# Kernel tuning notes

Hardware: AMD Instinct MI355X
Metric: run time of the kernel (lower is better)

The kernel has to match this reference:

```python
import jax, jax.numpy as jnp
import numpy as np

N_NODES = 50000
N_EDGES = 800000
VOCAB = 500
IN_DIM = 128
HID = 128
OUT_DIM = 64
N_GRAPHS = 512


def setup_inputs() -> dict:
    key = jax.random.key(0)
    ks = jax.random.split(key, 12)
    s = 0.05
    return {
        "emb": jax.random.normal(ks[0], (VOCAB, IN_DIM), jnp.float32) * s,
        "w1a": jax.random.normal(ks[1], (HID, IN_DIM), jnp.float32) * s,
        "b1a": jnp.zeros((HID,), jnp.float32),
        "w1b": jax.random.normal(ks[2], (HID, HID), jnp.float32) * s,
        "b1b": jnp.zeros((HID,), jnp.float32),
        "w2a": jax.random.normal(ks[3], (HID, HID), jnp.float32) * s,
        "b2a": jnp.zeros((HID,), jnp.float32),
        "w2b": jax.random.normal(ks[4], (HID, HID), jnp.float32) * s,
        "b2b": jnp.zeros((HID,), jnp.float32),
        "fc_w": jax.random.normal(ks[5], (OUT_DIM, HID), jnp.float32) * s,
        "fc_b": jnp.zeros((OUT_DIM,), jnp.float32),
        "x_idx": jax.random.randint(ks[6], (N_NODES,), 0, VOCAB, jnp.int32),
        "edge_index": jax.random.randint(ks[7], (2, N_EDGES), 0, N_NODES, jnp.int32),
        "batch": jnp.sort(jax.random.randint(ks[8], (N_NODES,), 0, N_GRAPHS, jnp.int32)),
    }


def gin_conv(x, wa, ba, wb, bb, src, dst):
    # GINConv with eps=0: MLP(x + sum_{j->i} x_j)
    agg = jax.ops.segment_sum(x[src], dst, num_segments=N_NODES)  # [N, d]
    h = x + agg
    h = jax.nn.relu(h @ wa.T + ba)
    return h @ wb.T + bb


def reference(emb, w1a, b1a, w1b, b1b, w2a, b2a, w2b, b2b, fc_w, fc_b,
              x_idx, edge_index, batch):
    src, dst = edge_index[0], edge_index[1]
    x = emb[x_idx]  # [N, IN_DIM] embedding lookup
    x = jax.nn.relu(gin_conv(x, w1a, b1a, w1b, b1b, src, dst))
    x = jax.nn.relu(gin_conv(x, w2a, b2a, w2b, b2b, src, dst))
    # global mean pool over graphs
    sums = jax.ops.segment_sum(x, batch, num_segments=N_GRAPHS)  # [G, HID]
    cnt = jax.ops.segment_sum(jnp.ones((N_NODES,), x.dtype), batch, num_segments=N_GRAPHS)
    pooled = sums / jnp.maximum(cnt, 1.0)[:, None]
    return pooled @ fc_w.T + fc_b  # [G, OUT_DIM]
```

## Files before the change

### kernel.cpp

```cpp
#include <hip/hip_runtime.h>

#define N_NODES 50000
#define N_EDGES 800000
#define DIM 128
#define NGRAPH 512
#define ODIM 64
#define VOCAB 500
#define NBKT 391
#define NB2 128
#define EPB2 (N_EDGES / NB2)
#define CAP 4096

typedef __attribute__((ext_vector_type(8))) short bf16x8;
typedef __attribute__((ext_vector_type(4))) short bf16x4;
typedef __attribute__((ext_vector_type(4))) float f32x4;

__device__ inline unsigned short f2bf(float f) {
  unsigned u = __builtin_bit_cast(unsigned, f);
  return (unsigned short)((u + 0x7fffu + ((u >> 16) & 1u)) >> 16);
}
__device__ inline float bf2f(unsigned short h) {
  unsigned u = ((unsigned)h) << 16;
  return __builtin_bit_cast(float, u);
}

__global__ __launch_bounds__(256) void prep_kernel(
    const float* __restrict__ emb,
    const float* __restrict__ w1a, const float* __restrict__ w1b,
    const float* __restrict__ w2a, const float* __restrict__ w2b,
    unsigned short* __restrict__ embb, unsigned short* __restrict__ wbf) {
  int u = blockIdx.x * 256 + threadIdx.x;
  const float* src;
  unsigned short* dst;
  if (u < VOCAB * 16) {
    src = emb + (size_t)u * 8;
    dst = embb + (size_t)u * 8;
  } else {
    int v = u - VOCAB * 16;
    if (v >= 4 * 2048) return;
    int m = v >> 11, loc = v & 2047;
    const float* w = (m == 0) ? w1a : (m == 1) ? w1b : (m == 2) ? w2a : w2b;
    src = w + (size_t)loc * 8;
    dst = wbf + (size_t)v * 8;
  }
  f32x4 a = ((const f32x4*)src)[0], b = ((const f32x4*)src)[1];
  bf16x8 o;
  #pragma unroll
  for (int e = 0; e < 4; ++e) {
    o[e] = (short)f2bf(a[e]);
    o[4 + e] = (short)f2bf(b[e]);
  }
  *(bf16x8*)dst = o;
}

__global__ __launch_bounds__(512) void bkt_hist_kernel(
    const int* __restrict__ ei, unsigned* __restrict__ HB) {
  __shared__ unsigned cnt[NBKT];
  int t = threadIdx.x, b = blockIdx.x;
  for (int i = t; i < NBKT; i += 512) cnt[i] = 0;
  __syncthreads();
  int base = b * EPB2;
  for (int i = t; i < EPB2; i += 512)
    atomicAdd(&cnt[(unsigned)ei[N_EDGES + base + i] >> 7], 1u);
  __syncthreads();
  for (int i = t; i < NBKT; i += 512) HB[(size_t)b * NBKT + i] = cnt[i];
}

__global__ __launch_bounds__(512) void bkt_scatter_kernel(
    const int* __restrict__ ei, const unsigned* __restrict__ HB,
    unsigned* __restrict__ eb) {
  __shared__ unsigned cur[NBKT];
  __shared__ unsigned wsum[8];
  int t = threadIdx.x, b = blockIdx.x;
  int lane = t & 63, wid = t >> 6;
  unsigned pre = 0, tot = 0;
  if (t < NBKT) {
    for (int bb = 0; bb < NB2; ++bb) {
      unsigned h = HB[(size_t)bb * NBKT + t];
      pre += (bb < b) ? h : 0u;
      tot += h;
    }
  }
  unsigned s = tot;
  #pragma unroll
  for (int d = 1; d < 64; d <<= 1) {
    unsigned u = __shfl_up(s, d, 64);
    if (lane >= d) s += u;
  }
  if (lane == 63) wsum[wid] = s;
  __syncthreads();
  if (wid == 0) {
    unsigned ws = (lane < 8) ? wsum[lane] : 0u;
    #pragma unroll
    for (int d = 1; d < 8; d <<= 1) {
      unsigned u = __shfl_up(ws, d, 64);
      if (lane >= d) ws += u;
    }
    if (lane < 8) wsum[lane] = ws;
  }
  __syncthreads();
  unsigned base = s - tot + (wid ? wsum[wid - 1] : 0u);
  if (t < NBKT) cur[t] = base + pre;
  __syncthreads();
  int ebase = b * EPB2;
  for (int i = t; i < EPB2; i += 512) {
    int sn = ei[ebase + i];
    unsigned d = (unsigned)ei[N_EDGES + ebase + i];
    unsigned pos = atomicAdd(&cur[d >> 7], 1u);
    eb[pos] = ((d & 127u) << 16) | (unsigned)sn;
  }
}

__global__ __launch_bounds__(512) void sort_bucket_kernel(
    const unsigned* __restrict__ HB, const unsigned* __restrict__ eb,
    int* __restrict__ srt, int* __restrict__ row) {
  __shared__ unsigned stage[CAP];
  __shared__ unsigned short sorted[CAP];
  __shared__ unsigned hist[128], cur[128];
  __shared__ unsigned wtot, wsum[8];
  __shared__ int sbound[2];
  int t = threadIdx.x, bkt = blockIdx.x;
  int lane = t & 63, wid = t >> 6;
  unsigned tot = 0;
  if (t < NBKT)
    for (int bb = 0; bb < NB2; ++bb) tot += HB[(size_t)bb * NBKT + t];
  unsigned s = tot;
  #pragma unroll
  for (int d = 1; d < 64; d <<= 1) {
    unsigned u = __shfl_up(s, d, 64);
    if (lane >= d) s += u;
  }
  if (lane == 63) wsum[wid] = s;
  __syncthreads();
  if (wid == 0) {
    unsigned ws = (lane < 8) ? wsum[lane] : 0u;
    #pragma unroll
    for (int d = 1; d < 8; d <<= 1) {
      unsigned u = __shfl_up(ws, d, 64);
      if (lane >= d) ws += u;
    }
    if (lane < 8) wsum[lane] = ws;
  }
  __syncthreads();
  unsigned base = s - tot + (wid ? wsum[wid - 1] : 0u);
  if (t == bkt) { sbound[0] = (int)base; sbound[1] = (int)(base + tot); }
  if (t < 128) hist[t] = 0;
  if (bkt == 0 && t == 0) row[N_NODES] = N_EDGES;
  __syncthreads();
  int bs = sbound[0];
  int cnt = sbound[1] - bs;
  if (cnt > CAP) cnt = CAP;
  for (int i = t; i < cnt; i += 512) {
    unsigned e = eb[bs + i];
    stage[i] = e;
    atomicAdd(&hist[e >> 16], 1u);
  }
  __syncthreads();
  if (t < 128) {
    unsigned v = hist[t], ss = v;
    #pragma unroll
    for (int d = 1; d < 64; d <<= 1) {
      unsigned u = __shfl_up(ss, d, 64);
      if (lane >= d) ss += u;
    }
    if (t == 63) wtot = ss;
    cur[t] = ss - v;
  }
  __syncthreads();
  if (t < 128) {
    unsigned e0 = cur[t] + (t >= 64 ? wtot : 0u);
    cur[t] = e0;
    int n = bkt * 128 + t;
    if (n < N_NODES) row[n] = bs + (int)e0;
  }
  __syncthreads();
  for (int i = t; i < cnt; i += 512) {
    unsigned e = stage[i];
    unsigned r = atomicAdd(&cur[e >> 16], 1u);
    sorted[r] = (unsigned short)(e & 0xFFFFu);
  }
  __syncthreads();
  for (int i = t; i < cnt; i += 512) srt[bs + i] = (int)sorted[i];
}

__global__ __launch_bounds__(256) void agg_emb_kernel(
    const unsigned short* __restrict__ embb, const int* __restrict__ xidx,
    const int* __restrict__ row, const int* __restrict__ srt,
    unsigned short* __restrict__ xa) {
  int n = blockIdx.x * 16 + (threadIdx.x >> 4);
  int c = threadIdx.x & 15;
  int lo = row[n], hi = row[n + 1];
  bf16x8 sv = *(const bf16x8*)(embb + (size_t)xidx[n] * DIM + c * 8);
  float a[8];
  #pragma unroll
  for (int e = 0; e < 8; ++e) a[e] = bf2f((unsigned short)sv[e]);
  int k = lo;
  for (; k + 8 <= hi; k += 8) {
    bf16x8 w[8];
    #pragma unroll
    for (int q = 0; q < 8; ++q)
      w[q] = *(const bf16x8*)(embb + (size_t)xidx[srt[k + q]] * DIM + c * 8);
    #pragma unroll
    for (int q = 0; q < 8; ++q)
      #pragma unroll
      for (int e = 0; e < 8; ++e) a[e] += bf2f((unsigned short)w[q][e]);
  }
  for (; k + 2 <= hi; k += 2) {
    bf16x8 w0 = *(const bf16x8*)(embb + (size_t)xidx[srt[k]] * DIM + c * 8);
    bf16x8 w1 = *(const bf16x8*)(embb + (size_t)xidx[srt[k + 1]] * DIM + c * 8);
    #pragma unroll
    for (int e = 0; e < 8; ++e)
      a[e] += bf2f((unsigned short)w0[e]) + bf2f((unsigned short)w1[e]);
  }
  if (k < hi) {
    bf16x8 w = *(const bf16x8*)(embb + (size_t)xidx[srt[k]] * DIM + c * 8);
    #pragma unroll
    for (int e = 0; e < 8; ++e) a[e] += bf2f((unsigned short)w[e]);
  }
  bf16x8 o;
  #pragma unroll
  for (int e = 0; e < 8; ++e) o[e] = (short)f2bf(a[e]);
  *(bf16x8*)(xa + (size_t)n * DIM + c * 8) = o;
}

__global__ __launch_bounds__(256) void agg_x_kernel(
    const unsigned short* __restrict__ x, const int* __restrict__ row,
    const int* __restrict__ srt, unsigned short* __restrict__ xa) {
  int n = blockIdx.x * 16 + (threadIdx.x >> 4);
  int c = threadIdx.x & 15;
  int lo = row[n], hi = row[n + 1];
  bf16x8 sv = *(const bf16x8*)(x + (size_t)n * DIM + c * 8);
  float a[8];
  #pragma unroll
  for (int e = 0; e < 8; ++e) a[e] = bf2f((unsigned short)sv[e]);
  int k = lo;
  for (; k + 8 <= hi; k += 8) {
    bf16x8 w[8];
    #pragma unroll
    for (int q = 0; q < 8; ++q)
      w[q] = *(const bf16x8*)(x + (size_t)srt[k + q] * DIM + c * 8);
    #pragma unroll
    for (int q = 0; q < 8; ++q)
      #pragma unroll
      for (int e = 0; e < 8; ++e) a[e] += bf2f((unsigned short)w[q][e]);
  }
  for (; k + 2 <= hi; k += 2) {
    bf16x8 w0 = *(const bf16x8*)(x + (size_t)srt[k] * DIM + c * 8);
    bf16x8 w1 = *(const bf16x8*)(x + (size_t)srt[k + 1] * DIM + c * 8);
    #pragma unroll
    for (int e = 0; e < 8; ++e)
      a[e] += bf2f((unsigned short)w0[e]) + bf2f((unsigned short)w1[e]);
  }
  if (k < hi) {
    bf16x8 w = *(const bf16x8*)(x + (size_t)srt[k] * DIM + c * 8);
    #pragma unroll
    for (int e = 0; e < 8; ++e) a[e] += bf2f((unsigned short)w[e]);
  }
  bf16x8 o;
  #pragma unroll
  for (int e = 0; e < 8; ++e) o[e] = (short)f2bf(a[e]);
  *(bf16x8*)(xa + (size_t)n * DIM + c * 8) = o;
}

__global__ __launch_bounds__(256) void mlp_mfma_kernel(
    const unsigned short* __restrict__ xa,
    const unsigned short* __restrict__ wabf, const float* __restrict__ ba,
    const unsigned short* __restrict__ wbbf, const float* __restrict__ bb,
    unsigned short* __restrict__ xout) {
  __shared__ short Xs[64 * 128];
  __shared__ short Hs[64 * 128];
  int t = threadIdx.x;
  int lane = t & 63;
  int w = t >> 6;
  int jq = w * 32;
  int l15 = lane & 15;
  int lg = lane >> 4;

  bf16x8 waf[2][4], wbf[2][4];
  #pragma unroll
  for (int jm = 0; jm < 2; ++jm) {
    int jrow = jq + jm * 16 + l15;
    #pragma unroll
    for (int ks = 0; ks < 4; ++ks) {
      int k0 = ks * 32 + lg * 8;
      waf[jm][ks] = *(const bf16x8*)(wabf + (size_t)jrow * DIM + k0);
      wbf[jm][ks] = *(const bf16x8*)(wbbf + (size_t)jrow * DIM + k0);
    }
  }
  f32x4 ba_r[2], bb_r[2];
  #pragma unroll
  for (int jm = 0; jm < 2; ++jm) {
    ba_r[jm] = *(const f32x4*)(ba + jq + jm * 16 + lg * 4);
    bb_r[jm] = *(const f32x4*)(bb + jq + jm * 16 + lg * 4);
  }

  for (int half = 0; half < 2; ++half) {
    int nbase = blockIdx.x * 128 + half * 64;

    {
      int r = t >> 2;
      int cb = (t & 3) * 4;
      int node = nbase + r;
      #pragma unroll
      for (int i = 0; i < 4; ++i) {
        int chunk = cb + i;
        bf16x8 v = {0, 0, 0, 0, 0, 0, 0, 0};
        if (node < N_NODES)
          v = *(const bf16x8*)(xa + (size_t)node * DIM + chunk * 8);
        *(bf16x8*)&Xs[r * 128 + ((chunk ^ (r & 7)) << 3)] = v;
      }
    }
    __syncthreads();

    #pragma unroll
    for (int nt = 0; nt < 4; ++nt) {
      int rrow = nt * 16 + l15;
      bf16x8 xf[4];
      #pragma unroll
      for (int ks = 0; ks < 4; ++ks) {
        int chunk = ks * 4 + lg;
        xf[ks] = *(const bf16x8*)&Xs[rrow * 128 + ((chunk ^ (rrow & 7)) << 3)];
      }
      #pragma unroll
      for (int jm = 0; jm < 2; ++jm) {
        f32x4 acc = ba_r[jm];
        #pragma unroll
        for (int ks = 0; ks < 4; ++ks)
          acc = __builtin_amdgcn_mfma_f32_16x16x32_bf16(waf[jm][ks], xf[ks], acc, 0, 0, 0);
        int hnode = nt * 16 + l15;
        int cbase = jq + jm * 16 + lg * 4;
        unsigned p0 = (unsigned)f2bf(fmaxf(acc[0], 0.f)) |
                      ((unsigned)f2bf(fmaxf(acc[1], 0.f)) << 16);
        unsigned p1 = (unsigned)f2bf(fmaxf(acc[2], 0.f)) |
                      ((unsigned)f2bf(fmaxf(acc[3], 0.f)) << 16);
        unsigned idx = hnode * 128 + (((cbase >> 3) ^ (hnode & 7)) << 3) + (cbase & 7);
        *(uint2*)&Hs[idx] = make_uint2(p0, p1);
      }
    }
    __syncthreads();

    #pragma unroll
    for (int nt = 0; nt < 4; ++nt) {
      int rrow = nt * 16 + l15;
      bf16x8 hf[4];
      #pragma unroll
      for (int ks = 0; ks < 4; ++ks) {
        int chunk = ks * 4 + lg;
        hf[ks] = *(const bf16x8*)&Hs[rrow * 128 + ((chunk ^ (rrow & 7)) << 3)];
      }
      #pragma unroll
      for (int jm = 0; jm < 2; ++jm) {
        f32x4 acc = bb_r[jm];
        #pragma unroll
        for (int ks = 0; ks < 4; ++ks)
          acc = __builtin_amdgcn_mfma_f32_16x16x32_bf16(wbf[jm][ks], hf[ks], acc, 0, 0, 0);
        int node = nbase + nt * 16 + l15;
        if (node < N_NODES) {
          bf16x4 o;
          #pragma unroll
          for (int e = 0; e < 4; ++e) o[e] = (short)f2bf(fmaxf(acc[e], 0.f));
          *(bf16x4*)(xout + (size_t)node * DIM + jq + jm * 16 + lg * 4) = o;
        }
      }
    }
    __syncthreads();
  }
}

#define PP 132
__global__ __launch_bounds__(256) void pool_fc_kernel(
    const unsigned short* __restrict__ x, const int* __restrict__ batch,
    const float* __restrict__ fcw, const float* __restrict__ fcb,
    float* __restrict__ out) {
  int g = blockIdx.x, t = threadIdx.x;
  __shared__ float part[16 * PP];
  __shared__ float pooled[DIM];
  __shared__ int sbound[2];
  if (t < 2) {
    int target = g + t;
    int lo = 0, hi = N_NODES;
    while (lo < hi) {
      int m = (lo + hi) >> 1;
      if (batch[m] < target) lo = m + 1; else hi = m;
    }
    sbound[t] = lo;
  }
  __syncthreads();
  int lo = sbound[0], hi = sbound[1];
  int r = t >> 4, c = t & 15;
  float acc[8] = {0.f, 0.f, 0.f, 0.f, 0.f, 0.f, 0.f, 0.f};
  for (int nn = lo + r; nn < hi; nn += 16) {
    bf16x8 v = *(const bf16x8*)(x + (size_t)nn * DIM + c * 8);
    #pragma unroll
    for (int e = 0; e < 8; ++e) acc[e] += bf2f((unsigned short)v[e]);
  }
  #pragma unroll
  for (int e = 0; e < 8; ++e) part[r * PP + c * 8 + e] = acc[e];
  __syncthreads();
  if (t < DIM) {
    float s = 0.f;
    #pragma unroll
    for (int rr = 0; rr < 16; ++rr) s += part[rr * PP + t];
    pooled[t] = s / fmaxf((float)(hi - lo), 1.0f);
  }
  __syncthreads();
  if (t < ODIM) {
    float a = fcb[t];
    const float* wr = fcw + (size_t)t * DIM;
    #pragma unroll 8
    for (int h = 0; h < DIM; ++h) a += pooled[h] * wr[h];
    out[(size_t)g * ODIM + t] = a;
  }
}

extern "C" void kernel_launch(void* const* d_in, const int* in_sizes, int n_in,
                              void* d_out, int out_size, void* d_ws, size_t ws_size,
                              hipStream_t stream) {
  const float* emb  = (const float*)d_in[0];
  const float* w1a  = (const float*)d_in[1];
  const float* b1a  = (const float*)d_in[2];
  const float* w1b  = (const float*)d_in[3];
  const float* b1b  = (const float*)d_in[4];
  const float* w2a  = (const float*)d_in[5];
  const float* b2a  = (const float*)d_in[6];
  const float* w2b  = (const float*)d_in[7];
  const float* b2b  = (const float*)d_in[8];
  const float* fcw  = (const float*)d_in[9];
  const float* fcb  = (const float*)d_in[10];
  const int*   xidx = (const int*)d_in[11];
  const int*   ei   = (const int*)d_in[12];
  const int*   batch= (const int*)d_in[13];
  float* out = (float*)d_out;

  size_t featb = (size_t)N_NODES * DIM * sizeof(unsigned short);
  char* ws = (char*)d_ws;
  unsigned short* B1 = (unsigned short*)ws;
  unsigned short* B2 = (unsigned short*)(ws + featb);
  char* p = ws + 2 * featb;
  unsigned short* embb = (unsigned short*)p;  p += (VOCAB * DIM * 2 + 15) / 16 * 16;
  unsigned short* wbf  = (unsigned short*)p;  p += (4 * DIM * DIM * 2 + 15) / 16 * 16;
  int* row  = (int*)p;      p += ((N_NODES + 1) * 4 + 15) / 16 * 16;
  unsigned* HB  = (unsigned*)p;  p += (size_t)NB2 * NBKT * 4;
  unsigned* eb  = (unsigned*)p;  p += (size_t)N_EDGES * 4;
  int* srt  = (int*)p;

  const unsigned short* w1abf = wbf;
  const unsigned short* w1bbf = wbf + DIM * DIM;
  const unsigned short* w2abf = wbf + 2 * DIM * DIM;
  const unsigned short* w2bbf = wbf + 3 * DIM * DIM;

  prep_kernel<<<(VOCAB * 16 + 4 * 2048 + 255) / 256, 256, 0, stream>>>(
      emb, w1a, w1b, w2a, w2b, embb, wbf);

  bkt_hist_kernel<<<NB2, 512, 0, stream>>>(ei, HB);
  bkt_scatter_kernel<<<NB2, 512, 0, stream>>>(ei, HB, eb);
  sort_bucket_kernel<<<NBKT, 512, 0, stream>>>(HB, eb, srt, row);

  agg_emb_kernel<<<N_NODES / 16, 256, 0, stream>>>(embb, xidx, row, srt, B1);
  mlp_mfma_kernel<<<(N_NODES + 127) / 128, 256, 0, stream>>>(B1, w1abf, b1a, w1bbf, b1b, B2);

  agg_x_kernel<<<N_NODES / 16, 256, 0, stream>>>(B2, row, srt, B1);
  mlp_mfma_kernel<<<(N_NODES + 127) / 128, 256, 0, stream>>>(B1, w2abf, b2a, w2bbf, b2b, B2);

  pool_fc_kernel<<<NGRAPH, 256, 0, stream>>>(B2, batch, fcw, fcb, out);
}
```

Baseline: 131.5 us.

## Fuse layer-1 aggregation into MLP kernel and precompute bucket bases

Merges the embedding-gather aggregation of the first GIN layer into a fused kernel that aggregates 128 nodes into shared memory and then runs both MFMA matmuls, which removes one feature-buffer write and reread plus a kernel launch. The bucket scatter kernel now writes the bucket prefix offsets so that the sort kernel no longer re-reads the whole histogram and redoes the scan in every block. The MLP kernel switches to 512 threads, with two halves of 4 waves each covering 128 rows at once instead of looping. In exchange, each block uses 64KB of shared memory, which may limit occupancy, and the fused gather phase only has 391 blocks for latency hiding.

```diff
diff --git a/kernel.cpp b/kernel.cpp
--- a/kernel.cpp
+++ b/kernel.cpp
@@ -68,7 +68,7 @@
 
 __global__ __launch_bounds__(512) void bkt_scatter_kernel(
     const int* __restrict__ ei, const unsigned* __restrict__ HB,
-    unsigned* __restrict__ eb) {
+    unsigned* __restrict__ eb, int* __restrict__ bktbase) {
   __shared__ unsigned cur[NBKT];
   __shared__ unsigned wsum[8];
   int t = threadIdx.x, b = blockIdx.x;
@@ -101,6 +101,10 @@
   __syncthreads();
   unsigned base = s - tot + (wid ? wsum[wid - 1] : 0u);
   if (t < NBKT) cur[t] = base + pre;
+  if (b == 0) {
+    if (t < NBKT) bktbase[t] = (int)base;
+    if (t == NBKT - 1) bktbase[NBKT] = (int)(base + tot);
+  }
   __syncthreads();
   int ebase = b * EPB2;
   for (int i = t; i < EPB2; i += 512) {
@@ -112,44 +116,19 @@
 }
 
 __global__ __launch_bounds__(512) void sort_bucket_kernel(
-    const unsigned* __restrict__ HB, const unsigned* __restrict__ eb,
+    const unsigned* __restrict__ eb, const int* __restrict__ bktbase,
     int* __restrict__ srt, int* __restrict__ row) {
   __shared__ unsigned stage[CAP];
   __shared__ unsigned short sorted[CAP];
   __shared__ unsigned hist[128], cur[128];
-  __shared__ unsigned wtot, wsum[8];
-  __shared__ int sbound[2];
+  __shared__ unsigned wtot;
   int t = threadIdx.x, bkt = blockIdx.x;
-  int lane = t & 63, wid = t >> 6;
-  unsigned tot = 0;
-  if (t < NBKT)
-    for (int bb = 0; bb < NB2; ++bb) tot += HB[(size_t)bb * NBKT + t];
-  unsigned s = tot;
-  #pragma unroll
-  for (int d = 1; d < 64; d <<= 1) {
-    unsigned u = __shfl_up(s, d, 64);
-    if (lane >= d) s += u;
-  }
-  if (lane == 63) wsum[wid] = s;
-  __syncthreads();
-  if (wid == 0) {
-    unsigned ws = (lane < 8) ? wsum[lane] : 0u;
-    #pragma unroll
-    for (int d = 1; d < 8; d <<= 1) {
-      unsigned u = __shfl_up(ws, d, 64);
-      if (lane >= d) ws += u;
-    }
-    if (lane < 8) wsum[lane] = ws;
-  }
-  __syncthreads();
-  unsigned base = s - tot + (wid ? wsum[wid - 1] : 0u);
-  if (t == bkt) { sbound[0] = (int)base; sbound[1] = (int)(base + tot); }
+  int bs = bktbase[bkt], be = bktbase[bkt + 1];
+  int cnt = be - bs;
+  if (cnt > CAP) cnt = CAP;
   if (t < 128) hist[t] = 0;
   if (bkt == 0 && t == 0) row[N_NODES] = N_EDGES;
   __syncthreads();
-  int bs = sbound[0];
-  int cnt = sbound[1] - bs;
-  if (cnt > CAP) cnt = CAP;
   for (int i = t; i < cnt; i += 512) {
     unsigned e = eb[bs + i];
     stage[i] = e;
@@ -157,6 +136,7 @@
   }
   __syncthreads();
   if (t < 128) {
+    int lane = t & 63;
     unsigned v = hist[t], ss = v;
     #pragma unroll
     for (int d = 1; d < 64; d <<= 1) {
@@ -183,44 +163,134 @@
   for (int i = t; i < cnt; i += 512) srt[bs + i] = (int)sorted[i];
 }
 
-__global__ __launch_bounds__(256) void agg_emb_kernel(
+__global__ __launch_bounds__(512) void conv1_kernel(
     const unsigned short* __restrict__ embb, const int* __restrict__ xidx,
     const int* __restrict__ row, const int* __restrict__ srt,
-    unsigned short* __restrict__ xa) {
-  int n = blockIdx.x * 16 + (threadIdx.x >> 4);
-  int c = threadIdx.x & 15;
-  int lo = row[n], hi = row[n + 1];
-  bf16x8 sv = *(const bf16x8*)(embb + (size_t)xidx[n] * DIM + c * 8);
-  float a[8];
-  #pragma unroll
-  for (int e = 0; e < 8; ++e) a[e] = bf2f((unsigned short)sv[e]);
-  int k = lo;
-  for (; k + 8 <= hi; k += 8) {
-    bf16x8 w[8];
-    #pragma unroll
-    for (int q = 0; q < 8; ++q)
-      w[q] = *(const bf16x8*)(embb + (size_t)xidx[srt[k + q]] * DIM + c * 8);
-    #pragma unroll
-    for (int q = 0; q < 8; ++q)
+    const unsigned short* __restrict__ wabf, const float* __restrict__ ba,
+    const unsigned short* __restrict__ wbbf, const float* __restrict__ bb,
+    unsigned short* __restrict__ xout) {
+  __shared__ short Xs[128 * 128];
+  __shared__ short Hs[128 * 128];
+  int t = threadIdx.x;
+  int lane = t & 63;
+  int w = t >> 6;
+  int half = w >> 2;
+  int jq = (w & 3) * 32;
+  int l15 = lane & 15;
+  int lg = lane >> 4;
+
+  bf16x8 waf[2][4], wbf[2][4];
+  #pragma unroll
+  for (int jm = 0; jm < 2; ++jm) {
+    int jrow = jq + jm * 16 + l15;
+    #pragma unroll
+    for (int ks = 0; ks < 4; ++ks) {
+      int k0 = ks * 32 + lg * 8;
+      waf[jm][ks] = *(const bf16x8*)(wabf + (size_t)jrow * DIM + k0);
+      wbf[jm][ks] = *(const bf16x8*)(wbbf + (size_t)jrow * DIM + k0);
+    }
+  }
+  f32x4 ba_r[2], bb_r[2];
+  #pragma unroll
+  for (int jm = 0; jm < 2; ++jm) {
+    ba_r[jm] = *(const f32x4*)(ba + jq + jm * 16 + lg * 4);
+    bb_r[jm] = *(const f32x4*)(bb + jq + jm * 16 + lg * 4);
+  }
+
+  {
+    int g = t >> 4;
+    int c = t & 15;
+    for (int i = 0; i < 4; ++i) {
+      int r = i * 32 + g;
+      int node = blockIdx.x * 128 + r;
+      float a[8] = {0.f, 0.f, 0.f, 0.f, 0.f, 0.f, 0.f, 0.f};
+      if (node < N_NODES) {
+        bf16x8 sv = *(const bf16x8*)(embb + (size_t)xidx[node] * DIM + c * 8);
+        #pragma unroll
+        for (int e = 0; e < 8; ++e) a[e] = bf2f((unsigned short)sv[e]);
+        int lo = row[node], hi = row[node + 1];
+        int k = lo;
+        for (; k + 8 <= hi; k += 8) {
+          bf16x8 wv[8];
+          #pragma unroll
+          for (int q = 0; q < 8; ++q)
+            wv[q] = *(const bf16x8*)(embb + (size_t)xidx[srt[k + q]] * DIM + c * 8);
+          #pragma unroll
+          for (int q = 0; q < 8; ++q)
+            #pragma unroll
+            for (int e = 0; e < 8; ++e) a[e] += bf2f((unsigned short)wv[q][e]);
+        }
+        for (; k + 2 <= hi; k += 2) {
+          bf16x8 w0 = *(const bf16x8*)(embb + (size_t)xidx[srt[k]] * DIM + c * 8);
+          bf16x8 w1 = *(const bf16x8*)(embb + (size_t)xidx[srt[k + 1]] * DIM + c * 8);
+          #pragma unroll
+          for (int e = 0; e < 8; ++e)
+            a[e] += bf2f((unsigned short)w0[e]) + bf2f((unsigned short)w1[e]);
+        }
+        if (k < hi) {
+          bf16x8 wv = *(const bf16x8*)(embb + (size_t)xidx[srt[k]] * DIM + c * 8);
+          #pragma unroll
+          for (int e = 0; e < 8; ++e) a[e] += bf2f((unsigned short)wv[e]);
+        }
+      }
+      bf16x8 o;
       #pragma unroll
-      for (int e = 0; e < 8; ++e) a[e] += bf2f((unsigned short)w[q][e]);
-  }
-  for (; k + 2 <= hi; k += 2) {
-    bf16x8 w0 = *(const bf16x8*)(embb + (size_t)xidx[srt[k]] * DIM + c * 8);
-    bf16x8 w1 = *(const bf16x8*)(embb + (size_t)xidx[srt[k + 1]] * DIM + c * 8);
-    #pragma unroll
-    for (int e = 0; e < 8; ++e)
-      a[e] += bf2f((unsigned short)w0[e]) + bf2f((unsigned short)w1[e]);
-  }
-  if (k < hi) {
-    bf16x8 w = *(const bf16x8*)(embb + (size_t)xidx[srt[k]] * DIM + c * 8);
-    #pragma unroll
-    for (int e = 0; e < 8; ++e) a[e] += bf2f((unsigned short)w[e]);
-  }
-  bf16x8 o;
-  #pragma unroll
-  for (int e = 0; e < 8; ++e) o[e] = (short)f2bf(a[e]);
-  *(bf16x8*)(xa + (size_t)n * DIM + c * 8) = o;
+      for (int e = 0; e < 8; ++e) o[e] = (short)f2bf(a[e]);
+      *(bf16x8*)&Xs[r * 128 + ((c ^ (r & 7)) << 3)] = o;
+    }
+  }
+  __syncthreads();
+
+  #pragma unroll
+  for (int nt = 0; nt < 4; ++nt) {
+    int rrow = half * 64 + nt * 16 + l15;
+    bf16x8 xf[4];
+    #pragma unroll
+    for (int ks = 0; ks < 4; ++ks) {
+      int chunk = ks * 4 + lg;
+      xf[ks] = *(const bf16x8*)&Xs[rrow * 128 + ((chunk ^ (rrow & 7)) << 3)];
+    }
+    #pragma unroll
+    for (int jm = 0; jm < 2; ++jm) {
+      f32x4 acc = ba_r[jm];
+      #pragma unroll
+      for (int ks = 0; ks < 4; ++ks)
+        acc = __builtin_amdgcn_mfma_f32_16x16x32_bf16(waf[jm][ks], xf[ks], acc, 0, 0, 0);
+      int cbase = jq + jm * 16 + lg * 4;
+      unsigned p0 = (unsigned)f2bf(fmaxf(acc[0], 0.f)) |
+                    ((unsigned)f2bf(fmaxf(acc[1], 0.f)) << 16);
+      unsigned p1 = (unsigned)f2bf(fmaxf(acc[2], 0.f)) |
+                    ((unsigned)f2bf(fmaxf(acc[3], 0.f)) << 16);
+      unsigned idx = rrow * 128 + (((cbase >> 3) ^ (rrow & 7)) << 3) + (cbase & 7);
+      *(uint2*)&Hs[idx] = make_uint2(p0, p1);
+    }
+  }
+  __syncthreads();
+
+  #pragma unroll
+  for (int nt = 0; nt < 4; ++nt) {
+    int rrow = half * 64 + nt * 16 + l15;
+    bf16x8 hf[4];
+    #pragma unroll
+    for (int ks = 0; ks < 4; ++ks) {
+      int chunk = ks * 4 + lg;
+      hf[ks] = *(const bf16x8*)&Hs[rrow * 128 + ((chunk ^ (rrow & 7)) << 3)];
+    }
+    #pragma unroll
+    for (int jm = 0; jm < 2; ++jm) {
+      f32x4 acc = bb_r[jm];
+      #pragma unroll
+      for (int ks = 0; ks < 4; ++ks)
+        acc = __builtin_amdgcn_mfma_f32_16x16x32_bf16(wbf[jm][ks], hf[ks], acc, 0, 0, 0);
+      int node = blockIdx.x * 128 + rrow;
+      if (node < N_NODES) {
+        bf16x4 o;
+        #pragma unroll
+        for (int e = 0; e < 4; ++e) o[e] = (short)f2bf(fmaxf(acc[e], 0.f));
+        *(bf16x4*)(xout + (size_t)node * DIM + jq + jm * 16 + lg * 4) = o;
+      }
+    }
+  }
 }
 
 __global__ __launch_bounds__(256) void agg_x_kernel(
@@ -262,17 +332,18 @@
   *(bf16x8*)(xa + (size_t)n * DIM + c * 8) = o;
 }
 
-__global__ __launch_bounds__(256) void mlp_mfma_kernel(
+__global__ __launch_bounds__(512) void mlp_mfma_kernel(
     const unsigned short* __restrict__ xa,
     const unsigned short* __restrict__ wabf, const float* __restrict__ ba,
     const unsigned short* __restrict__ wbbf, const float* __restrict__ bb,
     unsigned short* __restrict__ xout) {
-  __shared__ short Xs[64 * 128];
-  __shared__ short Hs[64 * 128];
+  __shared__ short Xs[128 * 128];
+  __shared__ short Hs[128 * 128];
   int t = threadIdx.x;
   int lane = t & 63;
   int w = t >> 6;
-  int jq = w * 32;
+  int half = w >> 2;
+  int jq = (w & 3) * 32;
   int l15 = lane & 15;
   int lg = lane >> 4;
 
@@ -294,76 +365,69 @@
     bb_r[jm] = *(const f32x4*)(bb + jq + jm * 16 + lg * 4);
   }
 
-  for (int half = 0; half < 2; ++half) {
-    int nbase = blockIdx.x * 128 + half * 64;
-
-    {
-      int r = t >> 2;
-      int cb = (t & 3) * 4;
-      int node = nbase + r;
+  {
+    #pragma unroll
+    for (int i = 0; i < 4; ++i) {
+      int unit = i * 512 + t;
+      int r = unit >> 4, chunk = unit & 15;
+      int node = blockIdx.x * 128 + r;
+      bf16x8 v = {0, 0, 0, 0, 0, 0, 0, 0};
+      if (node < N_NODES)
+        v = *(const bf16x8*)(xa + (size_t)node * DIM + chunk * 8);
+      *(bf16x8*)&Xs[r * 128 + ((chunk ^ (r & 7)) << 3)] = v;
+    }
+  }
+  __syncthreads();
+
+  #pragma unroll
+  for (int nt = 0; nt < 4; ++nt) {
+    int rrow = half * 64 + nt * 16 + l15;
+    bf16x8 xf[4];
+    #pragma unroll
+    for (int ks = 0; ks < 4; ++ks) {
+      int chunk = ks * 4 + lg;
+      xf[ks] = *(const bf16x8*)&Xs[rrow * 128 + ((chunk ^ (rrow & 7)) << 3)];
+    }
+    #pragma unroll
+    for (int jm = 0; jm < 2; ++jm) {
+      f32x4 acc = ba_r[jm];
       #pragma unroll
-      for (int i = 0; i < 4; ++i) {
-        int chunk = cb + i;
-        bf16x8 v = {0, 0, 0, 0, 0, 0, 0, 0};
-        if (node < N_NODES)
-          v = *(const bf16x8*)(xa + (size_t)node * DIM + chunk * 8);
-        *(bf16x8*)&Xs[r * 128 + ((chunk ^ (r & 7)) << 3)] = v;
+      for (int ks = 0; ks < 4; ++ks)
+        acc = __builtin_amdgcn_mfma_f32_16x16x32_bf16(waf[jm][ks], xf[ks], acc, 0, 0, 0);
+      int cbase = jq + jm * 16 + lg * 4;
+      unsigned p0 = (unsigned)f2bf(fmaxf(acc[0], 0.f)) |
+                    ((unsigned)f2bf(fmaxf(acc[1], 0.f)) << 16);
+      unsigned p1 = (unsigned)f2bf(fmaxf(acc[2], 0.f)) |
+                    ((unsigned)f2bf(fmaxf(acc[3], 0.f)) << 16);
+      unsigned idx = rrow * 128 + (((cbase >> 3) ^ (rrow & 7)) << 3) + (cbase & 7);
+      *(uint2*)&Hs[idx] = make_uint2(p0, p1);
+    }
+  }
+  __syncthreads();
+
+  #pragma unroll
+  for (int nt = 0; nt < 4; ++nt) {
+    int rrow = half * 64 + nt * 16 + l15;
+    bf16x8 hf[4];
+    #pragma unroll
+    for (int ks = 0; ks < 4; ++ks) {
+      int chunk = ks * 4 + lg;
+      hf[ks] = *(const bf16x8*)&Hs[rrow * 128 + ((chunk ^ (rrow & 7)) << 3)];
+    }
+    #pragma unroll
+    for (int jm = 0; jm < 2; ++jm) {
+      f32x4 acc = bb_r[jm];
+      #pragma unroll
+      for (int ks = 0; ks < 4; ++ks)
+        acc = __builtin_amdgcn_mfma_f32_16x16x32_bf16(wbf[jm][ks], hf[ks], acc, 0, 0, 0);
+      int node = blockIdx.x * 128 + rrow;
+      if (node < N_NODES) {
+        bf16x4 o;
+        #pragma unroll
+        for (int e = 0; e < 4; ++e) o[e] = (short)f2bf(fmaxf(acc[e], 0.f));
+        *(bf16x4*)(xout + (size_t)node * DIM + jq + jm * 16 + lg * 4) = o;
       }
     }
-    __syncthreads();
-
-    #pragma unroll
-    for (int nt = 0; nt < 4; ++nt) {
-      int rrow = nt * 16 + l15;
-      bf16x8 xf[4];
-      #pragma unroll
-      for (int ks = 0; ks < 4; ++ks) {
-        int chunk = ks * 4 + lg;
-        xf[ks] = *(const bf16x8*)&Xs[rrow * 128 + ((chunk ^ (rrow & 7)) << 3)];
-      }
-      #pragma unroll
-      for (int jm = 0; jm < 2; ++jm) {
-        f32x4 acc = ba_r[jm];
-        #pragma unroll
-        for (int ks = 0; ks < 4; ++ks)
-          acc = __builtin_amdgcn_mfma_f32_16x16x32_bf16(waf[jm][ks], xf[ks], acc, 0, 0, 0);
-        int hnode = nt * 16 + l15;
-        int cbase = jq + jm * 16 + lg * 4;
-        unsigned p0 = (unsigned)f2bf(fmaxf(acc[0], 0.f)) |
-                      ((unsigned)f2bf(fmaxf(acc[1], 0.f)) << 16);
-        unsigned p1 = (unsigned)f2bf(fmaxf(acc[2], 0.f)) |
-                      ((unsigned)f2bf(fmaxf(acc[3], 0.f)) << 16);
-        unsigned idx = hnode * 128 + (((cbase >> 3) ^ (hnode & 7)) << 3) + (cbase & 7);
-        *(uint2*)&Hs[idx] = make_uint2(p0, p1);
-      }
-    }
-    __syncthreads();
-
-    #pragma unroll
-    for (int nt = 0; nt < 4; ++nt) {
-      int rrow = nt * 16 + l15;
-      bf16x8 hf[4];
-      #pragma unroll
-      for (int ks = 0; ks < 4; ++ks) {
-        int chunk = ks * 4 + lg;
-        hf[ks] = *(const bf16x8*)&Hs[rrow * 128 + ((chunk ^ (rrow & 7)) << 3)];
-      }
-      #pragma unroll
-      for (int jm = 0; jm < 2; ++jm) {
-        f32x4 acc = bb_r[jm];
-        #pragma unroll
-        for (int ks = 0; ks < 4; ++ks)
-          acc = __builtin_amdgcn_mfma_f32_16x16x32_bf16(wbf[jm][ks], hf[ks], acc, 0, 0, 0);
-        int node = nbase + nt * 16 + l15;
-        if (node < N_NODES) {
-          bf16x4 o;
-          #pragma unroll
-          for (int e = 0; e < 4; ++e) o[e] = (short)f2bf(fmaxf(acc[e], 0.f));
-          *(bf16x4*)(xout + (size_t)node * DIM + jq + jm * 16 + lg * 4) = o;
-        }
-      }
-    }
-    __syncthreads();
   }
 }
 
@@ -440,6 +504,7 @@
   unsigned short* embb = (unsigned short*)p;  p += (VOCAB * DIM * 2 + 15) / 16 * 16;
   unsigned short* wbf  = (unsigned short*)p;  p += (4 * DIM * DIM * 2 + 15) / 16 * 16;
   int* row  = (int*)p;      p += ((N_NODES + 1) * 4 + 15) / 16 * 16;
+  int* bktbase = (int*)p;   p += ((NBKT + 1) * 4 + 15) / 16 * 16;
   unsigned* HB  = (unsigned*)p;  p += (size_t)NB2 * NBKT * 4;
   unsigned* eb  = (unsigned*)p;  p += (size_t)N_EDGES * 4;
   int* srt  = (int*)p;
@@ -453,14 +518,14 @@
       emb, w1a, w1b, w2a, w2b, embb, wbf);
 
   bkt_hist_kernel<<<NB2, 512, 0, stream>>>(ei, HB);
-  bkt_scatter_kernel<<<NB2, 512, 0, stream>>>(ei, HB, eb);
-  sort_bucket_kernel<<<NBKT, 512, 0, stream>>>(HB, eb, srt, row);
-
-  agg_emb_kernel<<<N_NODES / 16, 256, 0, stream>>>(embb, xidx, row, srt, B1);
-  mlp_mfma_kernel<<<(N_NODES + 127) / 128, 256, 0, stream>>>(B1, w1abf, b1a, w1bbf, b1b, B2);
+  bkt_scatter_kernel<<<NB2, 512, 0, stream>>>(ei, HB, eb, bktbase);
+  sort_bucket_kernel<<<NBKT, 512, 0, stream>>>(eb, bktbase, srt, row);
+
+  conv1_kernel<<<(N_NODES + 127) / 128, 512, 0, stream>>>(
+      embb, xidx, row, srt, w1abf, b1a, w1bbf, b1b, B2);
 
   agg_x_kernel<<<N_NODES / 16, 256, 0, stream>>>(B2, row, srt, B1);
-  mlp_mfma_kernel<<<(N_NODES + 127) / 128, 256, 0, stream>>>(B1, w2abf, b2a, w2bbf, b2b, B2);
+  mlp_mfma_kernel<<<(N_NODES + 127) / 128, 512, 0, stream>>>(B1, w2abf, b2a, w2bbf, b2b, B2);
 
   pool_fc_kernel<<<NGRAPH, 256, 0, stream>>>(B2, batch, fcw, fcb, out);
 }
```

After: 148.8 us. 1.13x slower.
